# Kernel tuning notes

Hardware: AMD Instinct MI355X
Metric: run time of the kernel (lower is better)

The kernel has to match this reference:

```python
import jax, jax.numpy as jnp
import numpy as np

C = 512
EPS = 1e-5


def _layer_norm(x, gamma, beta):
    mu = jnp.mean(x, axis=-1, keepdims=True)
    var = jnp.var(x, axis=-1, keepdims=True)
    return (x - mu) * jax.lax.rsqrt(var + EPS) * gamma + beta


def setup_inputs() -> dict:
    key = jax.random.key(0)
    ks = jax.random.split(key, 12)
    B, L = 8, 2048
    s = 1.0 / np.sqrt(C)
    return {
        "x1": jax.random.normal(ks[0], (B, C, L), dtype=jnp.float32),
        "x2": jax.random.normal(ks[1], (B, C, L), dtype=jnp.float32),
        "w_q": jax.random.normal(ks[2], (C, C), dtype=jnp.float32) * s,
        "b_q": jax.random.normal(ks[3], (C,), dtype=jnp.float32) * s,
        "w_k": jax.random.normal(ks[4], (C, C), dtype=jnp.float32) * s,
        "b_k": jax.random.normal(ks[5], (C,), dtype=jnp.float32) * s,
        "w_v1": jax.random.normal(ks[6], (C, C), dtype=jnp.float32) * s,
        "b_v1": jax.random.normal(ks[7], (C,), dtype=jnp.float32) * s,
        "w_v2": jax.random.normal(ks[8], (C, C), dtype=jnp.float32) * s,
        "b_v2": jax.random.normal(ks[9], (C,), dtype=jnp.float32) * s,
        "ln_gamma": jnp.ones((C,), dtype=jnp.float32),
        "ln_beta": jnp.zeros((C,), dtype=jnp.float32),
    }


def reference(x1, x2, w_q, b_q, w_k, b_k, w_v1, b_v1, w_v2, b_v2, ln_gamma, ln_beta):
    # (B, C, L) -> (B, L, C)
    x1 = jnp.swapaxes(x1, 1, 2)
    x2 = jnp.swapaxes(x2, 1, 2)
    # torch Linear: y = x @ W^T + b
    q = jnp.einsum("blc,dc->bld", x1, w_q) + b_q
    k = jnp.einsum("blc,dc->bld", x2, w_k) + b_k
    v1 = jnp.einsum("blc,dc->bld", x1, w_v1) + b_v1
    v2 = jnp.einsum("blc,dc->bld", x2, w_v2) + b_v2
    # shared attention scores [B, L1, L2]
    attn = jnp.einsum("bqc,bkc->bqk", q, k) / jnp.sqrt(jnp.float32(C))
    attn_k = jax.nn.softmax(attn, axis=-1)          # rows (over L2)
    attn_q = jax.nn.softmax(attn, axis=1)           # cols (over L1)
    vk = jnp.einsum("bqk,bkc->bqc", attn_k, v2)     # [B, L1, C]
    vq = jnp.einsum("bqk,bqc->bkc", attn_q, v1)     # [B, L2, C]
    # cross skip + shared layernorm
    r1 = _layer_norm(vk + x1, ln_gamma, ln_beta)
    r2 = _layer_norm(vq + x2, ln_gamma, ln_beta)
    return (jnp.swapaxes(r1, 1, 2), jnp.swapaxes(r2, 1, 2))
```

## Files before the change

kernel.cpp:

```cpp
#include <hip/hip_runtime.h>

#define L_DIM 2048
#define C_DIM 512
#define B_DIM 8

typedef __attribute__((ext_vector_type(8))) short bf16x8;
typedef __attribute__((ext_vector_type(4))) float f32x4;

constexpr size_t SQ  = (size_t)L_DIM * C_DIM;
constexpr size_t SAT = (size_t)L_DIM * L_DIM;
constexpr size_t MC  = (size_t)B_DIM * L_DIM * C_DIM;

__device__ __forceinline__ float bf2f(ushort u) {
  union { float f; unsigned int i; } c; c.i = ((unsigned int)u) << 16; return c.f;
}
__device__ __forceinline__ ushort f2bf(float f) {
  union { float f; unsigned int i; } c; c.f = f;
  unsigned int lsb = (c.i >> 16) & 1u;
  return (ushort)((c.i + 0x7FFFu + lsb) >> 16);
}

__device__ __forceinline__ float wave_red_max(float v) {
  #pragma unroll
  for (int o = 1; o < 64; o <<= 1) v = fmaxf(v, __shfl_xor(v, o, 64));
  return v;
}
__device__ __forceinline__ float wave_red_sum(float v) {
  #pragma unroll
  for (int o = 1; o < 64; o <<= 1) v += __shfl_xor(v, o, 64);
  return v;
}

__device__ __forceinline__ void glds16(const ushort* g, ushort* l) {
  __builtin_amdgcn_global_load_lds(
      (const __attribute__((address_space(1))) void*)g,
      (__attribute__((address_space(3))) void*)l, 16, 0, 0);
}

__device__ __forceinline__ int slotAB(int r, int c) {
  return (((c ^ (r & 7)) + (r >> 3)) & 7);
}
__device__ __forceinline__ int chAB(int r, int sl) {
  return ((sl - (r >> 3)) & 7) ^ (r & 7);
}
__device__ __forceinline__ int slotC(int r, int q4) {
  return ((q4 ^ (r & 15)) + (r >> 4)) & 15;
}

__device__ __forceinline__ int xcd_swz(int bid, int nwg) {
  return (bid & 7) * (nwg >> 3) + (bid >> 3);
}

__device__ __forceinline__ void gemm_core128(
    const ushort* __restrict__ Ab, const ushort* __restrict__ Bb,
    const float* __restrict__ bias,
    ushort* __restrict__ obN, ushort* __restrict__ obT,
    const int K, const int lda, const int ldb, const int ldo, const int ldoT,
    const int m0, const int n0, const float scale, const int EPI)
{
  __shared__ __align__(16) ushort lds[16384];

  const int t = threadIdx.x;
  const int lane = t & 63, w = t >> 6;
  const int wr = w >> 1, wc = w & 1;
  const int l16 = lane & 15, lhi = lane >> 4;
  const int lrow = lane >> 3, lsl = lane & 7;

  ushort* As = lds;
  ushort* Bs = lds + 8192;

  f32x4 acc[4][4];
  #pragma unroll
  for (int i = 0; i < 4; ++i)
    #pragma unroll
    for (int j = 0; j < 4; ++j) { f32x4 zv = {0.f, 0.f, 0.f, 0.f}; acc[i][j] = zv; }

  const int KT = K >> 6;
  for (int kt = 0; kt < KT; ++kt) {
    const int k0 = kt << 6;
    __syncthreads();
    #pragma unroll
    for (int p = 0; p < 4; ++p) {
      const int rbase = w * 32 + p * 8;
      const int rr = rbase + lrow;
      const int ch = chAB(rr, lsl);
      glds16(Ab + (size_t)(m0 + rr) * lda + k0 + ch * 8, As + rbase * 64);
      glds16(Bb + (size_t)(n0 + rr) * ldb + k0 + ch * 8, Bs + rbase * 64);
    }
    __syncthreads();
    #pragma unroll
    for (int ks = 0; ks < 2; ++ks) {
      bf16x8 af[4], bg[4];
      #pragma unroll
      for (int i = 0; i < 4; ++i) {
        const int ra = wr * 64 + i * 16 + l16;
        af[i] = *(const bf16x8*)&As[ra * 64 + 8 * slotAB(ra, ks * 4 + lhi)];
        const int rb = wc * 64 + i * 16 + l16;
        bg[i] = *(const bf16x8*)&Bs[rb * 64 + 8 * slotAB(rb, ks * 4 + lhi)];
      }
      #pragma unroll
      for (int i = 0; i < 4; ++i)
        #pragma unroll
        for (int j = 0; j < 4; ++j)
          acc[i][j] = __builtin_amdgcn_mfma_f32_16x16x32_bf16(af[i], bg[j], acc[i][j], 0, 0, 0);
    }
  }

  __syncthreads();
  ushort* Cs = lds;
  #pragma unroll
  for (int i = 0; i < 4; ++i) {
    #pragma unroll
    for (int j = 0; j < 4; ++j) {
      const int er = wr * 64 + i * 16 + lhi * 4;
      const int ec = wc * 64 + j * 16 + l16;
      const float bv = bias ? bias[n0 + ec] : 0.f;
      #pragma unroll
      for (int r = 0; r < 4; ++r) {
        const int rr = er + r;
        const float val = acc[i][j][r] * scale + bv;
        Cs[rr * 128 + 8 * slotC(rr, ec >> 3) + (ec & 7)] = f2bf(val);
      }
    }
  }
  __syncthreads();
  if (EPI == 0 || EPI == 2) {
    #pragma unroll
    for (int p = 0; p < 8; ++p) {
      const int id = p * 256 + t, r = id >> 4, cc = id & 15;
      const bf16x8 v = *(const bf16x8*)&Cs[r * 128 + 8 * slotC(r, cc)];
      *(bf16x8*)(obN + (size_t)(m0 + r) * ldo + n0 + cc * 8) = v;
    }
  }
  if (EPI >= 1) {
    #pragma unroll
    for (int p = 0; p < 8; ++p) {
      const int id = p * 256 + t, c = id >> 4, rs = id & 15;
      bf16x8 tv;
      #pragma unroll
      for (int jj = 0; jj < 8; ++jj) {
        const int r2 = rs * 8 + jj;
        tv[jj] = (short)Cs[r2 * 128 + 8 * slotC(r2, c >> 3) + (c & 7)];
      }
      *(bf16x8*)(obT + (size_t)(n0 + c) * ldoT + m0 + rs * 8) = tv;
    }
  }
}

__global__ __launch_bounds__(256, 4) void gemm_proj(
    const ushort* __restrict__ x1T, const ushort* __restrict__ x2T,
    const ushort* __restrict__ wbf,
    const float* __restrict__ b_q, const float* __restrict__ b_k,
    const float* __restrict__ b_v1, const float* __restrict__ b_v2,
    ushort* __restrict__ q, ushort* __restrict__ kb,
    ushort* __restrict__ v1T, ushort* __restrict__ v2T)
{
  const int lid = xcd_swz(blockIdx.x, 2048);
  const int x = lid & 15, y = (lid >> 4) & 3, rest = lid >> 6;
  const int b = rest & 7, pj = rest >> 3;
  const ushort* A = ((pj & 1) ? x2T : x1T) + (size_t)b * SQ;
  const ushort* B = wbf + (size_t)pj * (C_DIM * C_DIM);
  const float* bias = pj == 0 ? b_q : pj == 1 ? b_k : pj == 2 ? b_v1 : b_v2;
  if (pj < 2) {
    ushort* oN = (pj == 0 ? q : kb) + (size_t)b * SQ;
    gemm_core128(A, B, bias, oN, nullptr, C_DIM, C_DIM, C_DIM, C_DIM, 0,
                 x * 128, y * 128, 1.0f, 0);
  } else {
    ushort* oT = (pj == 2 ? v1T : v2T) + (size_t)b * SQ;
    gemm_core128(A, B, bias, nullptr, oT, C_DIM, C_DIM, C_DIM, 0, L_DIM,
                 x * 128, y * 128, 1.0f, 1);
  }
}

__global__ __launch_bounds__(256, 4) void gemm_qkt(
    const ushort* __restrict__ qb, const ushort* __restrict__ kb,
    ushort* __restrict__ attn, ushort* __restrict__ attnT, const float scale)
{
  const int lid = xcd_swz(blockIdx.x, 2048);
  const int x = lid & 15, y = (lid >> 4) & 15, b = lid >> 8;
  gemm_core128(qb + (size_t)b * SQ, kb + (size_t)b * SQ, nullptr,
               attn + (size_t)b * SAT, attnT + (size_t)b * SAT,
               C_DIM, C_DIM, C_DIM, L_DIM, L_DIM,
               x * 128, y * 128, scale, 2);
}

__global__ __launch_bounds__(256, 4) void gemm_pv(
    const ushort* __restrict__ attn, const ushort* __restrict__ attnT,
    const ushort* __restrict__ v1T, const ushort* __restrict__ v2T,
    ushort* __restrict__ vk, ushort* __restrict__ vq)
{
  const int lid = xcd_swz(blockIdx.x, 1024);
  const int x = lid & 15, y = (lid >> 4) & 3, rest = lid >> 6;
  const int which = rest & 1, b = rest >> 1;
  const ushort* A = (which ? attnT : attn) + (size_t)b * SAT;
  const ushort* B = (which ? v1T : v2T) + (size_t)b * SQ;
  ushort* o = (which ? vq : vk) + (size_t)b * SQ;
  gemm_core128(A, B, nullptr, o, nullptr,
               L_DIM, L_DIM, L_DIM, C_DIM, 0,
               x * 128, y * 128, 1.0f, 0);
}

__global__ __launch_bounds__(256) void softmax_rows(ushort* __restrict__ attn,
                                                    ushort* __restrict__ attnT)
{
  __shared__ float red[8];
  const int b = blockIdx.y, qi = blockIdx.x, t = threadIdx.x;
  ushort* base = blockIdx.z ? attnT : attn;
  ushort* row = base + ((size_t)b * L_DIM + qi) * L_DIM;
  bf16x8 v = *(const bf16x8*)&row[t * 8];
  float f[8];
  #pragma unroll
  for (int j = 0; j < 8; ++j) f[j] = bf2f((ushort)v[j]);
  float m = f[0];
  #pragma unroll
  for (int j = 1; j < 8; ++j) m = fmaxf(m, f[j]);
  m = wave_red_max(m);
  if ((t & 63) == 0) red[t >> 6] = m;
  __syncthreads();
  m = fmaxf(fmaxf(red[0], red[1]), fmaxf(red[2], red[3]));
  float s = 0.f;
  #pragma unroll
  for (int j = 0; j < 8; ++j) { f[j] = __expf(f[j] - m); s += f[j]; }
  s = wave_red_sum(s);
  if ((t & 63) == 0) red[4 + (t >> 6)] = s;
  __syncthreads();
  const float inv = 1.0f / (red[4] + red[5] + red[6] + red[7]);
  bf16x8 o;
  #pragma unroll
  for (int j = 0; j < 8; ++j) o[j] = (short)f2bf(f[j] * inv);
  *(bf16x8*)&row[t * 8] = o;
}

__global__ __launch_bounds__(256) void xpose(const float* __restrict__ x1,
                                             const float* __restrict__ x2,
                                             ushort* __restrict__ xT)
{
  __shared__ float s[64][65];
  const int z = blockIdx.z, l0 = blockIdx.x * 64, c0 = blockIdx.y * 64;
  const int t = threadIdx.x;
  const float* xb = (z < 8 ? x1 : x2) + ((size_t)(z & 7) * C_DIM + c0) * L_DIM + l0;
  #pragma unroll
  for (int p = 0; p < 16; ++p) {
    const int c = p * 4 + (t >> 6);
    s[c][t & 63] = xb[(size_t)c * L_DIM + (t & 63)];
  }
  __syncthreads();
  ushort* ob = xT + (size_t)z * SQ + (size_t)l0 * C_DIM + c0;
  #pragma unroll
  for (int p = 0; p < 16; ++p) {
    const int l = p * 4 + (t >> 6);
    ob[(size_t)l * C_DIM + (t & 63)] = f2bf(s[t & 63][l]);
  }
}

__global__ __launch_bounds__(256) void cvtw4(const float* __restrict__ a,
    const float* __restrict__ b, const float* __restrict__ c,
    const float* __restrict__ d, ushort* __restrict__ o)
{
  const int i = blockIdx.x * 256 + threadIdx.x;
  const int sel = i >> 18;
  const float* w = sel == 0 ? a : sel == 1 ? b : sel == 2 ? c : d;
  o[i] = f2bf(w[i & 262143]);
}

__global__ __launch_bounds__(256) void ln_out(const ushort* __restrict__ vk,
    const ushort* __restrict__ vq, const float* __restrict__ x1,
    const float* __restrict__ x2, const float* __restrict__ gamma,
    const float* __restrict__ beta, float* __restrict__ out)
{
  __shared__ float s[16][513];
  __shared__ float mu[16], rsd[16];
  __shared__ float gb[512], bb[512];
  const int t = threadIdx.x;
  const int b = blockIdx.y, l0 = blockIdx.x * 16, which = blockIdx.z;
  const ushort* vx = which ? vq : vk;
  const float* xo = which ? x2 : x1;
  float* obase = out + (size_t)which * MC;
  #pragma unroll
  for (int r = 0; r < 2; ++r) { gb[r * 256 + t] = gamma[r * 256 + t]; bb[r * 256 + t] = beta[r * 256 + t]; }
  const ushort* vb = vx + ((size_t)b * L_DIM + l0) * C_DIM;
  #pragma unroll
  for (int p = 0; p < 4; ++p) {
    const int id = p * 256 + t;
    const int l = id >> 6, cb = (id & 63) * 8;
    bf16x8 v = *(const bf16x8*)&vb[(size_t)l * C_DIM + cb];
    #pragma unroll
    for (int j = 0; j < 8; ++j) s[l][cb + j] = bf2f((ushort)v[j]);
  }
  __syncthreads();
  const float* xb = xo + (size_t)b * C_DIM * L_DIM + l0;
  for (int it = 0; it < 32; ++it) {
    const int idx = it * 256 + t, c = idx >> 4, l = idx & 15;
    s[l][c] += xb[(size_t)c * L_DIM + l];
  }
  __syncthreads();
  const int w = t >> 6, lane = t & 63;
  #pragma unroll
  for (int rr = 0; rr < 4; ++rr) {
    const int l = w * 4 + rr;
    float sum = 0.f, sq = 0.f;
    #pragma unroll
    for (int c0 = 0; c0 < 512; c0 += 64) {
      const float v = s[l][c0 + lane];
      sum += v; sq = fmaf(v, v, sq);
    }
    sum = wave_red_sum(sum); sq = wave_red_sum(sq);
    if (lane == 0) {
      const float m = sum * (1.f / 512.f);
      const float var = sq * (1.f / 512.f) - m * m;
      mu[l] = m; rsd[l] = rsqrtf(var + 1e-5f);
    }
  }
  __syncthreads();
  float* ob = obase + (size_t)b * C_DIM * L_DIM + l0;
  for (int it = 0; it < 32; ++it) {
    const int idx = it * 256 + t, c = idx >> 4, l = idx & 15;
    const float v = (s[l][c] - mu[l]) * rsd[l] * gb[c] + bb[c];
    ob[(size_t)c * L_DIM + l] = v;
  }
}

extern "C" void kernel_launch(void* const* d_in, const int* in_sizes, int n_in,
                              void* d_out, int out_size, void* d_ws, size_t ws_size,
                              hipStream_t stream) {
  const float* x1   = (const float*)d_in[0];
  const float* x2   = (const float*)d_in[1];
  const float* w_q  = (const float*)d_in[2];
  const float* b_q  = (const float*)d_in[3];
  const float* w_k  = (const float*)d_in[4];
  const float* b_k  = (const float*)d_in[5];
  const float* w_v1 = (const float*)d_in[6];
  const float* b_v1 = (const float*)d_in[7];
  const float* w_v2 = (const float*)d_in[8];
  const float* b_v2 = (const float*)d_in[9];
  const float* gamma= (const float*)d_in[10];
  const float* beta = (const float*)d_in[11];
  float* out = (float*)d_out;

  ushort* q    = (ushort*)d_ws;
  ushort* kbuf = q + MC;
  ushort* v1T  = kbuf + MC;
  ushort* v2T  = v1T + MC;
  ushort* attn = v2T + MC;
  ushort* x1T = attn;
  ushort* wbf = attn + 2 * MC;
  ushort* vkbuf = kbuf;
  ushort* vqbuf = q;
  ushort* attnT = (ushort*)d_out;

  const float iscale = 0.044194173824159216f;
  const dim3 blk256(256);

  cvtw4<<<4096, blk256, 0, stream>>>(w_q, w_k, w_v1, w_v2, wbf);
  xpose<<<dim3(32, 8, 16), blk256, 0, stream>>>(x1, x2, x1T);
  gemm_proj<<<2048, blk256, 0, stream>>>(x1T, x1T + MC, wbf,
      b_q, b_k, b_v1, b_v2, q, kbuf, v1T, v2T);
  gemm_qkt<<<2048, blk256, 0, stream>>>(q, kbuf, attn, attnT, iscale);
  softmax_rows<<<dim3(L_DIM, B_DIM, 2), blk256, 0, stream>>>(attn, attnT);
  gemm_pv<<<1024, blk256, 0, stream>>>(attn, attnT, v1T, v2T, vkbuf, vqbuf);
  ln_out<<<dim3(L_DIM / 16, B_DIM, 2), blk256, 0, stream>>>(
      vkbuf, vqbuf, x1, x2, gamma, beta, out);
}
```

Measured before the change: 285.0 us.

## Fuse softmax into QK^T epilogue stats and PV prologue exponentiation

Removes the standalone softmax kernel, which read and wrote both attention matrices. The QK^T GEMM epilogue now computes per-tile row and column max/sum partials, a small combine kernel reduces them, and the PV GEMM applies exp(x - max) while loading A into LDS and scales by 1/sum in its epilogue. This avoids a full read-modify-write pass over the 2x8x2048x2048 bf16 attention buffers. In exchange, the A operand in PV now goes through register loads with exp work instead of direct global-to-LDS loads, and the exp is recomputed for every N tile.

```diff
diff --git a/kernel.cpp b/kernel.cpp
--- a/kernel.cpp
+++ b/kernel.cpp
@@ -10,6 +10,14 @@
 constexpr size_t SQ  = (size_t)L_DIM * C_DIM;
 constexpr size_t SAT = (size_t)L_DIM * L_DIM;
 constexpr size_t MC  = (size_t)B_DIM * L_DIM * C_DIM;
+constexpr int BL = B_DIM * L_DIM;
+
+__device__ float g_pmr[16][BL];
+__device__ float g_psr[16][BL];
+__device__ float g_pmc[16][BL];
+__device__ float g_psc[16][BL];
+__device__ float g_statm[2][BL];
+__device__ float g_stati[2][BL];
 
 __device__ __forceinline__ float bf2f(ushort u) {
   union { float f; unsigned int i; } c; c.i = ((unsigned int)u) << 16; return c.f;
@@ -20,11 +28,6 @@
   return (ushort)((c.i + 0x7FFFu + lsb) >> 16);
 }
 
-__device__ __forceinline__ float wave_red_max(float v) {
-  #pragma unroll
-  for (int o = 1; o < 64; o <<= 1) v = fmaxf(v, __shfl_xor(v, o, 64));
-  return v;
-}
 __device__ __forceinline__ float wave_red_sum(float v) {
   #pragma unroll
   for (int o = 1; o < 64; o <<= 1) v += __shfl_xor(v, o, 64);
@@ -51,14 +54,17 @@
   return (bid & 7) * (nwg >> 3) + (bid >> 3);
 }
 
+template <bool STATS, bool SOFT>
 __device__ __forceinline__ void gemm_core128(
     const ushort* __restrict__ Ab, const ushort* __restrict__ Bb,
     const float* __restrict__ bias,
     ushort* __restrict__ obN, ushort* __restrict__ obT,
     const int K, const int lda, const int ldb, const int ldo, const int ldoT,
-    const int m0, const int n0, const float scale, const int EPI)
+    const int m0, const int n0, const float scale, const int EPI,
+    const int sb, const float* __restrict__ statm, const float* __restrict__ stati)
 {
   __shared__ __align__(16) ushort lds[16384];
+  __shared__ float smx[128], sinv[128];
 
   const int t = threadIdx.x;
   const int lane = t & 63, w = t >> 6;
@@ -69,6 +75,10 @@
   ushort* As = lds;
   ushort* Bs = lds + 8192;
 
+  if (SOFT) {
+    if (t < 128) { smx[t] = statm[t]; sinv[t] = stati[t]; }
+  }
+
   f32x4 acc[4][4];
   #pragma unroll
   for (int i = 0; i < 4; ++i)
@@ -79,13 +89,34 @@
   for (int kt = 0; kt < KT; ++kt) {
     const int k0 = kt << 6;
     __syncthreads();
-    #pragma unroll
-    for (int p = 0; p < 4; ++p) {
-      const int rbase = w * 32 + p * 8;
-      const int rr = rbase + lrow;
-      const int ch = chAB(rr, lsl);
-      glds16(Ab + (size_t)(m0 + rr) * lda + k0 + ch * 8, As + rbase * 64);
-      glds16(Bb + (size_t)(n0 + rr) * ldb + k0 + ch * 8, Bs + rbase * 64);
+    if (SOFT) {
+      #pragma unroll
+      for (int p = 0; p < 4; ++p) {
+        const int rbase = w * 32 + p * 8;
+        const int rr = rbase + lrow;
+        const int ch = chAB(rr, lsl);
+        glds16(Bb + (size_t)(n0 + rr) * ldb + k0 + ch * 8, Bs + rbase * 64);
+      }
+      #pragma unroll
+      for (int p = 0; p < 4; ++p) {
+        const int rr = w * 32 + p * 8 + lrow;
+        const bf16x8 va = *(const bf16x8*)(Ab + (size_t)(m0 + rr) * lda + k0 + lsl * 8);
+        const float mx = smx[rr];
+        bf16x8 tv;
+        #pragma unroll
+        for (int j = 0; j < 8; ++j)
+          tv[j] = (short)f2bf(__expf(bf2f((ushort)va[j]) - mx));
+        *(bf16x8*)&As[rr * 64 + 8 * slotAB(rr, lsl)] = tv;
+      }
+    } else {
+      #pragma unroll
+      for (int p = 0; p < 4; ++p) {
+        const int rbase = w * 32 + p * 8;
+        const int rr = rbase + lrow;
+        const int ch = chAB(rr, lsl);
+        glds16(Ab + (size_t)(m0 + rr) * lda + k0 + ch * 8, As + rbase * 64);
+        glds16(Bb + (size_t)(n0 + rr) * ldb + k0 + ch * 8, Bs + rbase * 64);
+      }
     }
     __syncthreads();
     #pragma unroll
@@ -118,7 +149,8 @@
       #pragma unroll
       for (int r = 0; r < 4; ++r) {
         const int rr = er + r;
-        const float val = acc[i][j][r] * scale + bv;
+        float val = acc[i][j][r] * scale + bv;
+        if (SOFT) val *= sinv[rr];
         Cs[rr * 128 + 8 * slotC(rr, ec >> 3) + (ec & 7)] = f2bf(val);
       }
     }
@@ -143,6 +175,42 @@
         tv[jj] = (short)Cs[r2 * 128 + 8 * slotC(r2, c >> 3) + (c & 7)];
       }
       *(bf16x8*)(obT + (size_t)(n0 + c) * ldoT + m0 + rs * 8) = tv;
+    }
+  }
+
+  if (STATS) {
+    if (t < 128) {
+      const int r = t;
+      float m = -1e30f, s = 0.f;
+      #pragma unroll
+      for (int cc = 0; cc < 16; ++cc) {
+        const bf16x8 v8 = *(const bf16x8*)&Cs[r * 128 + 8 * slotC(r, cc)];
+        float f[8];
+        #pragma unroll
+        for (int j = 0; j < 8; ++j) f[j] = bf2f((ushort)v8[j]);
+        float mx = f[0];
+        #pragma unroll
+        for (int j = 1; j < 8; ++j) mx = fmaxf(mx, f[j]);
+        const float nm = fmaxf(m, mx);
+        float add = 0.f;
+        #pragma unroll
+        for (int j = 0; j < 8; ++j) add += __expf(f[j] - nm);
+        s = s * __expf(m - nm) + add;
+        m = nm;
+      }
+      g_pmr[n0 >> 7][sb * L_DIM + m0 + r] = m;
+      g_psr[n0 >> 7][sb * L_DIM + m0 + r] = s;
+    } else {
+      const int c = t - 128;
+      float m = -1e30f, s = 0.f;
+      #pragma unroll 8
+      for (int r2 = 0; r2 < 128; ++r2) {
+        const float v = bf2f(Cs[r2 * 128 + 8 * slotC(r2, c >> 3) + (c & 7)]);
+        if (v > m) { s = s * __expf(m - v) + 1.f; m = v; }
+        else       { s += __expf(v - m); }
+      }
+      g_pmc[m0 >> 7][sb * L_DIM + n0 + c] = m;
+      g_psc[m0 >> 7][sb * L_DIM + n0 + c] = s;
     }
   }
 }
@@ -163,12 +231,12 @@
   const float* bias = pj == 0 ? b_q : pj == 1 ? b_k : pj == 2 ? b_v1 : b_v2;
   if (pj < 2) {
     ushort* oN = (pj == 0 ? q : kb) + (size_t)b * SQ;
-    gemm_core128(A, B, bias, oN, nullptr, C_DIM, C_DIM, C_DIM, C_DIM, 0,
-                 x * 128, y * 128, 1.0f, 0);
+    gemm_core128<false, false>(A, B, bias, oN, nullptr, C_DIM, C_DIM, C_DIM,
+                               C_DIM, 0, x * 128, y * 128, 1.0f, 0, 0, nullptr, nullptr);
   } else {
     ushort* oT = (pj == 2 ? v1T : v2T) + (size_t)b * SQ;
-    gemm_core128(A, B, bias, nullptr, oT, C_DIM, C_DIM, C_DIM, 0, L_DIM,
-                 x * 128, y * 128, 1.0f, 1);
+    gemm_core128<false, false>(A, B, bias, nullptr, oT, C_DIM, C_DIM, C_DIM,
+                               0, L_DIM, x * 128, y * 128, 1.0f, 1, 0, nullptr, nullptr);
   }
 }
 
@@ -178,10 +246,26 @@
 {
   const int lid = xcd_swz(blockIdx.x, 2048);
   const int x = lid & 15, y = (lid >> 4) & 15, b = lid >> 8;
-  gemm_core128(qb + (size_t)b * SQ, kb + (size_t)b * SQ, nullptr,
+  gemm_core128<true, false>(qb + (size_t)b * SQ, kb + (size_t)b * SQ, nullptr,
                attn + (size_t)b * SAT, attnT + (size_t)b * SAT,
                C_DIM, C_DIM, C_DIM, L_DIM, L_DIM,
-               x * 128, y * 128, scale, 2);
+               x * 128, y * 128, scale, 2, b, nullptr, nullptr);
+}
+
+__global__ __launch_bounds__(256) void sm_combine()
+{
+  const int i = blockIdx.x * 256 + threadIdx.x;
+  const int which = blockIdx.y;
+  const float* pm = which ? &g_pmc[0][0] : &g_pmr[0][0];
+  const float* ps = which ? &g_psc[0][0] : &g_psr[0][0];
+  float m = -1e30f;
+  #pragma unroll
+  for (int p = 0; p < 16; ++p) m = fmaxf(m, pm[p * BL + i]);
+  float s = 0.f;
+  #pragma unroll
+  for (int p = 0; p < 16; ++p) s += ps[p * BL + i] * __expf(pm[p * BL + i] - m);
+  g_statm[which][i] = m;
+  g_stati[which][i] = 1.0f / s;
 }
 
 __global__ __launch_bounds__(256, 4) void gemm_pv(
@@ -195,40 +279,11 @@
   const ushort* A = (which ? attnT : attn) + (size_t)b * SAT;
   const ushort* B = (which ? v1T : v2T) + (size_t)b * SQ;
   ushort* o = (which ? vq : vk) + (size_t)b * SQ;
-  gemm_core128(A, B, nullptr, o, nullptr,
+  const int m0 = x * 128;
+  gemm_core128<false, true>(A, B, nullptr, o, nullptr,
                L_DIM, L_DIM, L_DIM, C_DIM, 0,
-               x * 128, y * 128, 1.0f, 0);
-}
-
-__global__ __launch_bounds__(256) void softmax_rows(ushort* __restrict__ attn,
-                                                    ushort* __restrict__ attnT)
-{
-  __shared__ float red[8];
-  const int b = blockIdx.y, qi = blockIdx.x, t = threadIdx.x;
-  ushort* base = blockIdx.z ? attnT : attn;
-  ushort* row = base + ((size_t)b * L_DIM + qi) * L_DIM;
-  bf16x8 v = *(const bf16x8*)&row[t * 8];
-  float f[8];
-  #pragma unroll
-  for (int j = 0; j < 8; ++j) f[j] = bf2f((ushort)v[j]);
-  float m = f[0];
-  #pragma unroll
-  for (int j = 1; j < 8; ++j) m = fmaxf(m, f[j]);
-  m = wave_red_max(m);
-  if ((t & 63) == 0) red[t >> 6] = m;
-  __syncthreads();
-  m = fmaxf(fmaxf(red[0], red[1]), fmaxf(red[2], red[3]));
-  float s = 0.f;
-  #pragma unroll
-  for (int j = 0; j < 8; ++j) { f[j] = __expf(f[j] - m); s += f[j]; }
-  s = wave_red_sum(s);
-  if ((t & 63) == 0) red[4 + (t >> 6)] = s;
-  __syncthreads();
-  const float inv = 1.0f / (red[4] + red[5] + red[6] + red[7]);
-  bf16x8 o;
-  #pragma unroll
-  for (int j = 0; j < 8; ++j) o[j] = (short)f2bf(f[j] * inv);
-  *(bf16x8*)&row[t * 8] = o;
+               m0, y * 128, 1.0f, 0, b,
+               &g_statm[which][b * L_DIM + m0], &g_stati[which][b * L_DIM + m0]);
 }
 
 __global__ __launch_bounds__(256) void xpose(const float* __restrict__ x1,
@@ -356,7 +411,7 @@
   gemm_proj<<<2048, blk256, 0, stream>>>(x1T, x1T + MC, wbf,
       b_q, b_k, b_v1, b_v2, q, kbuf, v1T, v2T);
   gemm_qkt<<<2048, blk256, 0, stream>>>(q, kbuf, attn, attnT, iscale);
-  softmax_rows<<<dim3(L_DIM, B_DIM, 2), blk256, 0, stream>>>(attn, attnT);
+  sm_combine<<<dim3(BL / 256, 2), blk256, 0, stream>>>();
   gemm_pv<<<1024, blk256, 0, stream>>>(attn, attnT, v1T, v2T, vkbuf, vqbuf);
   ln_out<<<dim3(L_DIM / 16, B_DIM, 2), blk256, 0, stream>>>(
       vkbuf, vqbuf, x1, x2, gamma, beta, out);
```

Result: slower. 334.9 us (+17.5%).
